# Kernel optimization log

Measured on AMD Instinct MI355X. Metric: run time of the kernel, lower is better.

## Reference

```python
import jax, jax.numpy as jnp
import numpy as np

A, B, M, H, NMOL = 100000, 200000, 50000, 128, 4000
DEPTH = 5
MAX_NB = 8


def setup_inputs() -> dict:
    key = jax.random.key(0)
    ks = jax.random.split(key, 10)
    fatoms = jax.random.normal(ks[0], (A, 35), dtype=jnp.float32)
    fbonds = jax.random.normal(ks[1], (B, 40), dtype=jnp.float32)
    # index 0 of the combined message table is the zero padding message
    tree_message = jax.random.normal(ks[2], (M, H), dtype=jnp.float32).at[0].set(0.0)
    agraph = jax.random.randint(ks[3], (A, MAX_NB), 0, M + B, dtype=jnp.int32)
    bgraph = jax.random.randint(ks[4], (B, MAX_NB), 0, M + B, dtype=jnp.int32)
    mol_id = jnp.sort(jax.random.randint(ks[5], (A,), 0, NMOL, dtype=jnp.int32))
    W_i = jax.random.normal(ks[6], (40, H), dtype=jnp.float32) * 0.05
    W_h = jax.random.normal(ks[7], (H, H), dtype=jnp.float32) * 0.05
    W_o = jax.random.normal(ks[8], (35 + H, H), dtype=jnp.float32) * 0.05
    b_o = jax.random.normal(ks[9], (H,), dtype=jnp.float32) * 0.05
    return {"fatoms": fatoms, "fbonds": fbonds, "tree_message": tree_message,
            "agraph": agraph, "bgraph": bgraph, "mol_id": mol_id,
            "W_i": W_i, "W_h": W_h, "W_o": W_o, "b_o": b_o, "n_mols": NMOL}


def reference(fatoms, fbonds, tree_message, agraph, bgraph, mol_id, W_i, W_h, W_o, b_o, n_mols):
    binput = fbonds @ W_i                      # [B, H]
    graph_message = jax.nn.relu(binput)        # [B, H]
    for _ in range(DEPTH - 1):
        message = jnp.concatenate([tree_message, graph_message], axis=0)  # [M+B, H]
        nei = jnp.take(message, bgraph, axis=0).sum(axis=1)               # [B, H]
        graph_message = jax.nn.relu(binput + nei @ W_h)
    message = jnp.concatenate([tree_message, graph_message], axis=0)
    nei_a = jnp.take(message, agraph, axis=0).sum(axis=1)                 # [A, H]
    ainput = jnp.concatenate([fatoms, nei_a], axis=1)                     # [A, 35+H]
    atom_hiddens = jax.nn.relu(ainput @ W_o + b_o)                        # [A, H]
    sums = jax.ops.segment_sum(atom_hiddens, mol_id, num_segments=n_mols)
    counts = jax.ops.segment_sum(jnp.ones((atom_hiddens.shape[0],), dtype=atom_hiddens.dtype),
                                 mol_id, num_segments=n_mols)
    mol_vecs = sums / jnp.maximum(counts, 1.0)[:, None]                   # [n_mols, H]
    return mol_vecs
```

## Files before the change

### kernel.cpp

```cpp
#include <hip/hip_runtime.h>
#include <hip/hip_bf16.h>

#define AN 100000
#define BN 200000
#define MN 50000
#define HD 128
#define NMOL 4000
#define MAXNB 8
#define BSZ 24576

typedef unsigned short u16;
typedef unsigned int   u32;
typedef unsigned char  u8;
typedef float f32x4 __attribute__((ext_vector_type(4)));
typedef float f32x2 __attribute__((ext_vector_type(2)));
typedef short s16x8 __attribute__((ext_vector_type(8)));

__device__ __forceinline__ u16 f2bf(float x) {
    u32 u = __float_as_uint(x);
    return (u16)((u + 0x7fffu + ((u >> 16) & 1u)) >> 16);
}
__device__ __forceinline__ float bf2f(u16 x) { return __uint_as_float((u32)x << 16); }

__device__ __forceinline__ s16x8 zero8() { return (s16x8){0, 0, 0, 0, 0, 0, 0, 0}; }

__device__ __forceinline__ s16x8 pack44(float4 a, float4 b) {
    union { uint4 u; s16x8 s; } r;
    r.u.x = (u32)f2bf(a.x) | ((u32)f2bf(a.y) << 16);
    r.u.y = (u32)f2bf(a.z) | ((u32)f2bf(a.w) << 16);
    r.u.z = (u32)f2bf(b.x) | ((u32)f2bf(b.y) << 16);
    r.u.w = (u32)f2bf(b.z) | ((u32)f2bf(b.w) << 16);
    return r.s;
}

#if defined(__has_builtin)
#if __has_builtin(__builtin_amdgcn_cvt_pk_f32_fp8) && __has_builtin(__builtin_amdgcn_cvt_pk_fp8_f32)
#define HW_FP8 1
#endif
#endif

__device__ __forceinline__ void fp8x4_to_f32(u32 w, float* o) {
#ifdef HW_FP8
    f32x2 a = __builtin_amdgcn_cvt_pk_f32_fp8((int)w, false);
    f32x2 b = __builtin_amdgcn_cvt_pk_f32_fp8((int)w, true);
    o[0] = a.x; o[1] = a.y; o[2] = b.x; o[3] = b.y;
#else
#pragma unroll
    for (int i = 0; i < 4; ++i) {
        u32 b8 = (w >> (i * 8)) & 0xffu;
        u32 s = (b8 >> 7) & 1u, em = b8 & 0x7fu;
        float v;
        if (em < 8u) v = (float)em * 0.001953125f;
        else v = __uint_as_float((((em >> 3) + 120u) << 23) | ((em & 7u) << 20));
        o[i] = s ? -v : v;
    }
#endif
}

__device__ __forceinline__ u32 f32_1_to_fp8_sw(float x) {
    u32 s = (__float_as_uint(x) >> 31) << 7;
    float ax = fabsf(x);
    if (ax >= 448.f) return s | 0x7e;
    u32 b = __float_as_uint(ax);
    int e = (int)(b >> 23) - 127;
    if (e < -6) {
        float t = ax * 512.0f;
        u32 m = (u32)(t + 0.5f);
        if (m > 8u) m = 8u;
        return s | m;
    }
    u32 mant = b & 0x7fffffu;
    u32 keep = mant >> 20;
    u32 rest = mant & 0xfffffu;
    u32 rnd = (rest > 0x80000u) || (rest == 0x80000u && (keep & 1u));
    keep += rnd;
    u32 ee = (u32)(e + 7);
    if (keep == 8u) { keep = 0u; ee++; }
    if (ee >= 16u || (ee == 15u && keep == 7u)) return s | 0x7e;
    return s | (ee << 3) | keep;
}

__device__ __forceinline__ u32 f32x4_to_fp8(float a, float b, float c, float d) {
#ifdef HW_FP8
    int r = __builtin_amdgcn_cvt_pk_fp8_f32(a, b, 0, false);
    r = __builtin_amdgcn_cvt_pk_fp8_f32(c, d, r, true);
    return (u32)r;
#else
    return f32_1_to_fp8_sw(a) | (f32_1_to_fp8_sw(b) << 8) |
           (f32_1_to_fp8_sw(c) << 16) | (f32_1_to_fp8_sw(d) << 24);
#endif
}

__global__ __launch_bounds__(256) void k_prep(const float* __restrict__ tree,
                                              u16* __restrict__ tree_bf,
                                              const float* __restrict__ W_h,
                                              const float* __restrict__ W_i,
                                              const float* __restrict__ W_o,
                                              const float* __restrict__ b_o,
                                              u16* __restrict__ Bit,
                                              u16* __restrict__ Bat,
                                              const int* __restrict__ mol_id,
                                              float* __restrict__ counts,
                                              const float* __restrict__ fbonds,
                                              u16* __restrict__ fbp,
                                              const int* __restrict__ bgraph,
                                              int* __restrict__ bgd,
                                              int bgd_end) {
    int blk = blockIdx.x, tid = threadIdx.x;
    if (blk < 6250) {
        int i = blk * 256 + tid;
        const float4 v = ((const float4*)tree)[i];
        uint2 r;
        r.x = (u32)f2bf(v.x) | ((u32)f2bf(v.y) << 16);
        r.y = (u32)f2bf(v.z) | ((u32)f2bf(v.w) << 16);
        ((uint2*)tree_bf)[i] = r;
    } else if (blk < 6442) {
        int i = (blk - 6250) * 256 + tid;
        int which = (i >= BSZ);
        int e = which ? i - BSZ : i;
        int j = e & 7, lane = (e >> 3) & 63, nt = (e >> 9) & 7, kt = e >> 12;
        int k = kt * 32 + (lane >> 4) * 8 + j;
        int n = nt * 16 + (lane & 15);
        if (!which) {
            float v = (k < 128) ? W_h[k * 128 + n] : ((k < 168) ? W_i[(k - 128) * 128 + n] : 0.f);
            Bit[e] = f2bf(v);
        } else {
            float v = (k < 128) ? W_o[(35 + k) * 128 + n]
                    : (k < 163) ? W_o[(k - 128) * 128 + n]
                    : (k == 163) ? b_o[n] : 0.f;
            Bat[e] = f2bf(v);
        }
    } else if (blk < 6458) {
        int m = (blk - 6442) * 256 + tid;
        if (m < NMOL) {
            int lo = 0, hi = AN;
            while (lo < hi) { int mid = (lo + hi) >> 1; if (mol_id[mid] < m) lo = mid + 1; else hi = mid; }
            int s = lo; lo = 0; hi = AN;
            while (lo < hi) { int mid = (lo + hi) >> 1; if (mol_id[mid] < m + 1) lo = mid + 1; else hi = mid; }
            counts[m] = (float)(lo - s);
        }
    } else if (blk < bgd_end) {
        int q = (blk - 6458) * 256 + tid;
        if (q < 400000) {
            int4 v = ((const int4*)bgraph)[q];
            v.x = (v.x >= MN) ? v.x : 0;
            v.y = (v.y >= MN) ? v.y : 0;
            v.z = (v.z >= MN) ? v.z : 0;
            v.w = (v.w >= MN) ? v.w : 0;
            ((int4*)bgd)[q] = v;
        }
    } else {
        int q = (blk - bgd_end) * 256 + tid;
        if (q < 2000000) {
            const float4 v = ((const float4*)fbonds)[q];
            uint2 r;
            r.x = (u32)f2bf(v.x) | ((u32)f2bf(v.y) << 16);
            r.y = (u32)f2bf(v.z) | ((u32)f2bf(v.w) << 16);
            ((uint2*)fbp)[q] = r;
        }
    }
}

#define LDA 136

__device__ __forceinline__ void fb_frags_pk(const u16* __restrict__ fbp, int b, int aq,
                                            s16x8& lo, s16x8& hi) {
    const uint4* f4 = (const uint4*)fbp;
    uint4 v = f4[(size_t)b * 5 + aq];
    lo = *(const s16x8*)&v;
    if (aq == 0) {
        uint4 w = f4[(size_t)b * 5 + 4];
        hi = *(const s16x8*)&w;
    } else hi = zero8();
}

__device__ __forceinline__ void fb_frags_f32(const float* __restrict__ fbonds, int b, int aq,
                                             s16x8& lo, s16x8& hi) {
    const float4* f4 = (const float4*)(fbonds + (size_t)b * 40);
    float4 x = f4[aq * 2], y = f4[aq * 2 + 1];
    lo = pack44(x, y);
    if (aq == 0) {
        float4 p = f4[8], q = f4[9];
        hi = pack44(p, q);
    } else hi = zero8();
}

__device__ __forceinline__ void acc_bf16(const uint4& v, float* a) {
    a[0] += __uint_as_float(v.x << 16);
    a[1] += __uint_as_float(v.x & 0xffff0000u);
    a[2] += __uint_as_float(v.y << 16);
    a[3] += __uint_as_float(v.y & 0xffff0000u);
    a[4] += __uint_as_float(v.z << 16);
    a[5] += __uint_as_float(v.z & 0xffff0000u);
    a[6] += __uint_as_float(v.w << 16);
    a[7] += __uint_as_float(v.w & 0xffff0000u);
}

__device__ __forceinline__ void pack_row(u16 (*sA)[LDA], int row, int l, const float* a) {
    uint4 r;
    r.x = (u32)f2bf(a[0]) | ((u32)f2bf(a[1]) << 16);
    r.y = (u32)f2bf(a[2]) | ((u32)f2bf(a[3]) << 16);
    r.z = (u32)f2bf(a[4]) | ((u32)f2bf(a[5]) << 16);
    r.w = (u32)f2bf(a[6]) | ((u32)f2bf(a[7]) << 16);
    *(uint4*)&sA[row][l * 8] = r;
}

__device__ __forceinline__ void gather16(u16 (*sA)[LDA], const int (*sidx)[MAXNB],
                                         const u16* __restrict__ tree_bf,
                                         const u16* __restrict__ tin, int tid) {
    int l = tid & 15, tb = tid >> 4;
#pragma unroll
    for (int pp = 0; pp < 2; ++pp) {
        int r0 = tb + (2 * pp) * 16;
        int r1 = tb + (2 * pp + 1) * 16;
        uint4 v[2][8];
#pragma unroll
        for (int j = 0; j < 8; ++j) {
            int idx = sidx[r0][j];
            const u16* base = (idx < MN) ? tree_bf + (size_t)idx * HD
                                         : tin + (size_t)(idx - MN) * HD;
            v[0][j] = ((const uint4*)base)[l];
        }
#pragma unroll
        for (int j = 0; j < 8; ++j) {
            int idx = sidx[r1][j];
            const u16* base = (idx < MN) ? tree_bf + (size_t)idx * HD
                                         : tin + (size_t)(idx - MN) * HD;
            v[1][j] = ((const uint4*)base)[l];
        }
#pragma unroll
        for (int h = 0; h < 2; ++h) {
            float a[8] = {0.f, 0.f, 0.f, 0.f, 0.f, 0.f, 0.f, 0.f};
#pragma unroll
            for (int j = 0; j < 8; ++j) acc_bf16(v[h][j], a);
            pack_row(sA, h == 0 ? r0 : r1, l, a);
        }
    }
}

__device__ __forceinline__ void gather_tree(u16 (*sA)[LDA], const int (*sidx)[MAXNB],
                                            const u16* __restrict__ tree_bf, int tid) {
    int l = tid & 15, tb = tid >> 4;
#pragma unroll
    for (int pp = 0; pp < 2; ++pp) {
        int r0 = tb + (2 * pp) * 16;
        int r1 = tb + (2 * pp + 1) * 16;
        uint4 v[2][8];
#pragma unroll
        for (int j = 0; j < 8; ++j) {
            int idx = sidx[r0][j];
            uint4 w = {0u, 0u, 0u, 0u};
            if (idx) w = ((const uint4*)(tree_bf + (size_t)idx * HD))[l];
            v[0][j] = w;
        }
#pragma unroll
        for (int j = 0; j < 8; ++j) {
            int idx = sidx[r1][j];
            uint4 w = {0u, 0u, 0u, 0u};
            if (idx) w = ((const uint4*)(tree_bf + (size_t)idx * HD))[l];
            v[1][j] = w;
        }
#pragma unroll
        for (int h = 0; h < 2; ++h) {
            float a[8] = {0.f, 0.f, 0.f, 0.f, 0.f, 0.f, 0.f, 0.f};
#pragma unroll
            for (int j = 0; j < 8; ++j) acc_bf16(v[h][j], a);
            pack_row(sA, h == 0 ? r0 : r1, l, a);
        }
    }
}

__device__ __forceinline__ void gather_fp8(u16 (*sA)[LDA], const int (*sidx)[MAXNB],
                                           const u8* __restrict__ tin, int tid) {
    int l = tid & 15, tb = tid >> 4;
#pragma unroll
    for (int pp = 0; pp < 2; ++pp) {
        int r0 = tb + (2 * pp) * 16;
        int r1 = tb + (2 * pp + 1) * 16;
        uint2 v[2][8];
#pragma unroll
        for (int j = 0; j < 8; ++j) {
            int idx = sidx[r0][j];
            uint2 w = {0u, 0u};
            if (idx) w = *((const uint2*)(tin + (size_t)(idx - MN) * HD) + l);
            v[0][j] = w;
        }
#pragma unroll
        for (int j = 0; j < 8; ++j) {
            int idx = sidx[r1][j];
            uint2 w = {0u, 0u};
            if (idx) w = *((const uint2*)(tin + (size_t)(idx - MN) * HD) + l);
            v[1][j] = w;
        }
#pragma unroll
        for (int h = 0; h < 2; ++h) {
            float a[8] = {0.f, 0.f, 0.f, 0.f, 0.f, 0.f, 0.f, 0.f};
#pragma unroll
            for (int j = 0; j < 8; ++j) {
                float t[4];
                fp8x4_to_f32(v[h][j].x, t);
                a[0] += t[0]; a[1] += t[1]; a[2] += t[2]; a[3] += t[3];
                fp8x4_to_f32(v[h][j].y, t);
                a[4] += t[0]; a[5] += t[1]; a[6] += t[2]; a[7] += t[3];
            }
            pack_row(sA, h == 0 ? r0 : r1, l, a);
        }
    }
}

__device__ __forceinline__ void gather_mixed(u16 (*sA)[LDA], const int (*sidx)[MAXNB],
                                             const u16* __restrict__ tree_bf,
                                             const u8* __restrict__ dyn, int tid) {
    int l = tid & 15, tb = tid >> 4;
#pragma unroll
    for (int pp = 0; pp < 4; ++pp) {
        int r = tb + pp * 16;
        uint4 v[8]; int id[8];
#pragma unroll
        for (int j = 0; j < 8; ++j) {
            int idx = sidx[r][j];
            id[j] = idx;
            uint4 w = {0u, 0u, 0u, 0u};
            if (idx >= MN) {
                uint2 t = *((const uint2*)(dyn + (size_t)(idx - MN) * HD) + l);
                w.x = t.x; w.y = t.y;
            } else if (idx) {
                w = ((const uint4*)(tree_bf + (size_t)idx * HD))[l];
            }
            v[j] = w;
        }
        float a[8] = {0.f, 0.f, 0.f, 0.f, 0.f, 0.f, 0.f, 0.f};
#pragma unroll
        for (int j = 0; j < 8; ++j) {
            if (id[j] >= MN) {
                float t[4];
                fp8x4_to_f32(v[j].x, t);
                a[0] += t[0]; a[1] += t[1]; a[2] += t[2]; a[3] += t[3];
                fp8x4_to_f32(v[j].y, t);
                a[4] += t[0]; a[5] += t[1]; a[6] += t[2]; a[7] += t[3];
            } else {
                acc_bf16(v[j], a);
            }
        }
        pack_row(sA, r, l, a);
    }
}

__device__ __forceinline__ void store_tile_fp8(const u16 (*sA)[LDA], u8* __restrict__ dst,
                                               int b0, int tid) {
#pragma unroll
    for (int s = 0; s < 4; ++s) {
        int e = tid + s * 256;
        int row = e >> 4, seg = e & 15;
        uint4 w = *(const uint4*)&sA[row][seg * 8];
        float f0 = fminf(__uint_as_float(w.x << 16), 448.f);
        float f1 = fminf(__uint_as_float(w.x & 0xffff0000u), 448.f);
        float f2 = fminf(__uint_as_float(w.y << 16), 448.f);
        float f3 = fminf(__uint_as_float(w.y & 0xffff0000u), 448.f);
        float f4 = fminf(__uint_as_float(w.z << 16), 448.f);
        float f5 = fminf(__uint_as_float(w.z & 0xffff0000u), 448.f);
        float f6 = fminf(__uint_as_float(w.w << 16), 448.f);
        float f7 = fminf(__uint_as_float(w.w & 0xffff0000u), 448.f);
        uint2 o;
        o.x = f32x4_to_fp8(f0, f1, f2, f3);
        o.y = f32x4_to_fp8(f4, f5, f6, f7);
        *((uint2*)(dst + (size_t)(b0 + row) * HD) + seg) = o;
    }
}

template <bool PK>
__global__ __launch_bounds__(256) void k_binput2(const float* __restrict__ fbonds,
                                                 const u16* __restrict__ fbp,
                                                 const u16* __restrict__ tree_bf,
                                                 const int* __restrict__ bgraph,
                                                 const u16* __restrict__ Bsw,
                                                 u8* __restrict__ g0,
                                                 u16* __restrict__ base2) {
    __shared__ __align__(16) u16 sA[64][LDA];
    __shared__ int sidx[64][MAXNB];
    int tid = threadIdx.x;
    int b0  = blockIdx.x * 64;

    for (int i = tid; i < 64 * MAXNB; i += 256) {
        int idx = bgraph[(size_t)(b0 + (i >> 3)) * MAXNB + (i & 7)];
        sidx[i >> 3][i & 7] = (idx < MN) ? idx : 0;
    }
    __syncthreads();
    gather_tree(sA, sidx, tree_bf, tid);
    __syncthreads();

    int lane = tid & 63, wv = tid >> 6;
    int am = lane & 15, aq = lane >> 4;
    s16x8 afr[6];
#pragma unroll
    for (int kt = 0; kt < 4; ++kt)
        afr[kt] = *(const s16x8*)&sA[wv * 16 + am][kt * 32 + aq * 8];
    int b = b0 + wv * 16 + am;
    if (PK) fb_frags_pk(fbp, b, aq, afr[4], afr[5]);
    else    fb_frags_f32(fbonds, b, aq, afr[4], afr[5]);

    const s16x8* B8 = (const s16x8*)Bsw;
    f32x4 acc[8];
#pragma unroll
    for (int nt = 0; nt < 8; ++nt) acc[nt] = (f32x4){0.f, 0.f, 0.f, 0.f};
#pragma unroll
    for (int kt = 4; kt < 6; ++kt)
#pragma unroll
        for (int nt = 0; nt < 8; ++nt) {
            s16x8 bfr = B8[(kt * 8 + nt) * 64 + lane];
            acc[nt] = __builtin_amdgcn_mfma_f32_16x16x32_bf16(afr[kt], bfr, acc[nt], 0, 0, 0);
        }
#pragma unroll
    for (int nt = 0; nt < 8; ++nt)
#pragma unroll
        for (int r = 0; r < 4; ++r)
            sA[wv * 16 + aq * 4 + r][nt * 16 + am] = f2bf(fmaxf(acc[nt][r], 0.f));
    __syncthreads();
    store_tile_fp8(sA, g0, b0, tid);
#pragma unroll
    for (int kt = 0; kt < 4; ++kt)
#pragma unroll
        for (int nt = 0; nt < 8; ++nt) {
            s16x8 bfr = B8[(kt * 8 + nt) * 64 + lane];
            acc[nt] = __builtin_amdgcn_mfma_f32_16x16x32_bf16(afr[kt], bfr, acc[nt], 0, 0, 0);
        }
    __syncthreads();
#pragma unroll
    for (int nt = 0; nt < 8; ++nt)
#pragma unroll
        for (int r = 0; r < 4; ++r)
            sA[wv * 16 + aq * 4 + r][nt * 16 + am] = f2bf(acc[nt][r]);
    __syncthreads();
#pragma unroll
    for (int s = 0; s < 4; ++s) {
        int e = tid + s * 256;
        int row = e >> 4, seg = e & 15;
        *(uint4*)&base2[((size_t)b0 + row) * HD + seg * 8] = *(const uint4*)&sA[row][seg * 8];
    }
}

__global__ __launch_bounds__(256) void k_iter_fold(const u8* __restrict__ tin,
                                                   const u16* __restrict__ base2,
                                                   const int* __restrict__ bgd,
                                                   const u16* __restrict__ Bsw,
                                                   u8* __restrict__ tout) {
    __shared__ __align__(16) u16 sA[64][LDA];
    __shared__ int sidx[64][MAXNB];
    int tid = threadIdx.x;
    int b0  = blockIdx.x * 64;

    for (int i = tid; i < 64 * MAXNB; i += 256)
        sidx[i >> 3][i & 7] = bgd[(size_t)(b0 + (i >> 3)) * MAXNB + (i & 7)];
    __syncthreads();

    gather_fp8(sA, sidx, tin, tid);

    int lane = tid & 63, wv = tid >> 6;
    int am = lane & 15, aq = lane >> 4;
    f32x4 acc[8];
    {
        const u16* b2 = base2 + (size_t)(b0 + wv * 16 + aq * 4) * HD + am;
#pragma unroll
        for (int r = 0; r < 4; ++r)
#pragma unroll
            for (int nt = 0; nt < 8; ++nt)
                acc[nt][r] = bf2f(b2[(size_t)r * HD + nt * 16]);
    }
    __syncthreads();

    s16x8 afr[4];
#pragma unroll
    for (int kt = 0; kt < 4; ++kt)
        afr[kt] = *(const s16x8*)&sA[wv * 16 + am][kt * 32 + aq * 8];
    const s16x8* B8 = (const s16x8*)Bsw;
#pragma unroll
    for (int kt = 0; kt < 4; ++kt)
#pragma unroll
        for (int nt = 0; nt < 8; ++nt) {
            s16x8 bfr = B8[(kt * 8 + nt) * 64 + lane];
            acc[nt] = __builtin_amdgcn_mfma_f32_16x16x32_bf16(afr[kt], bfr, acc[nt], 0, 0, 0);
        }
#pragma unroll
    for (int nt = 0; nt < 8; ++nt)
#pragma unroll
        for (int r = 0; r < 4; ++r)
            sA[wv * 16 + aq * 4 + r][nt * 16 + am] = f2bf(fmaxf(acc[nt][r], 0.f));
    __syncthreads();
    store_tile_fp8(sA, tout, b0, tid);
}

template <bool PK>
__global__ __launch_bounds__(256) void k_binput_mfma(const float* __restrict__ fbonds,
                                                     const u16* __restrict__ fbp,
                                                     const u16* __restrict__ Bsw,
                                                     u16* __restrict__ g0) {
    __shared__ __align__(16) u16 sA[64][LDA];
    int tid = threadIdx.x;
    int b0  = blockIdx.x * 64;
    int lane = tid & 63, wv = tid >> 6;
    int am = lane & 15, aq = lane >> 4;
    int b = b0 + wv * 16 + am;
    s16x8 afr[2];
    if (PK) fb_frags_pk(fbp, b, aq, afr[0], afr[1]);
    else    fb_frags_f32(fbonds, b, aq, afr[0], afr[1]);
    f32x4 acc[8];
#pragma unroll
    for (int nt = 0; nt < 8; ++nt) acc[nt] = (f32x4){0.f, 0.f, 0.f, 0.f};
    const s16x8* B8 = (const s16x8*)Bsw;
#pragma unroll
    for (int kt = 0; kt < 2; ++kt)
#pragma unroll
        for (int nt = 0; nt < 8; ++nt) {
            s16x8 bfr = B8[((4 + kt) * 8 + nt) * 64 + lane];
            acc[nt] = __builtin_amdgcn_mfma_f32_16x16x32_bf16(afr[kt], bfr, acc[nt], 0, 0, 0);
        }
#pragma unroll
    for (int nt = 0; nt < 8; ++nt)
#pragma unroll
        for (int r = 0; r < 4; ++r)
            sA[wv * 16 + aq * 4 + r][nt * 16 + am] = f2bf(fmaxf(acc[nt][r], 0.f));
    __syncthreads();
#pragma unroll
    for (int s = 0; s < 4; ++s) {
        int e = tid + s * 256;
        int row = e >> 4, seg = e & 15;
        *(uint4*)&g0[((size_t)b0 + row) * HD + seg * 8] = *(const uint4*)&sA[row][seg * 8];
    }
}

template <bool PK>
__global__ __launch_bounds__(256) void k_iter_mfma(const u16* __restrict__ tree_bf,
                                                   const u16* __restrict__ tin,
                                                   const float* __restrict__ fbonds,
                                                   const u16* __restrict__ fbp,
                                                   const int* __restrict__ bgraph,
                                                   const u16* __restrict__ Bsw,
                                                   u16* __restrict__ tout) {
    __shared__ __align__(16) u16 sA[64][LDA];
    __shared__ int sidx[64][MAXNB];
    int tid = threadIdx.x;
    int b0  = blockIdx.x * 64;

    for (int i = tid; i < 64 * MAXNB; i += 256)
        sidx[i >> 3][i & 7] = bgraph[(size_t)(b0 + (i >> 3)) * MAXNB + (i & 7)];
    __syncthreads();

    gather16(sA, sidx, tree_bf, tin, tid);
    __syncthreads();

    int lane = tid & 63, wv = tid >> 6;
    int am = lane & 15, aq = lane >> 4;
    s16x8 afr[6];
#pragma unroll
    for (int kt = 0; kt < 4; ++kt)
        afr[kt] = *(const s16x8*)&sA[wv * 16 + am][kt * 32 + aq * 8];
    int b = b0 + wv * 16 + am;
    if (PK) fb_frags_pk(fbp, b, aq, afr[4], afr[5]);
    else    fb_frags_f32(fbonds, b, aq, afr[4], afr[5]);
    f32x4 acc[8];
#pragma unroll
    for (int nt = 0; nt < 8; ++nt) acc[nt] = (f32x4){0.f, 0.f, 0.f, 0.f};
    const s16x8* B8 = (const s16x8*)Bsw;
#pragma unroll
    for (int kt = 0; kt < 6; ++kt)
#pragma unroll
        for (int nt = 0; nt < 8; ++nt) {
            s16x8 bfr = B8[(kt * 8 + nt) * 64 + lane];
            acc[nt] = __builtin_amdgcn_mfma_f32_16x16x32_bf16(afr[kt], bfr, acc[nt], 0, 0, 0);
        }
#pragma unroll
    for (int nt = 0; nt < 8; ++nt)
#pragma unroll
        for (int r = 0; r < 4; ++r)
            sA[wv * 16 + aq * 4 + r][nt * 16 + am] = f2bf(fmaxf(acc[nt][r], 0.f));
    __syncthreads();
#pragma unroll
    for (int s = 0; s < 4; ++s) {
        int e = tid + s * 256;
        int row = e >> 4, seg = e & 15;
        *(uint4*)&tout[((size_t)b0 + row) * HD + seg * 8] = *(const uint4*)&sA[row][seg * 8];
    }
}

template <bool F8>
__global__ __launch_bounds__(256) void k_atom_mfma(const u16* __restrict__ tree_bf,
                                                   const void* __restrict__ gfin,
                                                   const float* __restrict__ fatoms,
                                                   const int* __restrict__ agraph,
                                                   const int* __restrict__ mol_id,
                                                   const u16* __restrict__ Bsw,
                                                   float* __restrict__ sums) {
    __shared__ __align__(16) u16 sA[64][LDA];
    __shared__ int sidx[64][MAXNB];
    __shared__ int smol[64];
    int tid = threadIdx.x;
    int a0  = blockIdx.x * 64;

    for (int i = tid; i < 64 * MAXNB; i += 256) {
        int a = a0 + (i >> 3);
        sidx[i >> 3][i & 7] = (a < AN) ? agraph[(size_t)a * MAXNB + (i & 7)] : 0;
    }
    if (tid < 64) smol[tid] = (a0 + tid < AN) ? mol_id[a0 + tid] : -1;
    __syncthreads();
    if (F8) gather_mixed(sA, sidx, tree_bf, (const u8*)gfin, tid);
    else    gather16(sA, sidx, tree_bf, (const u16*)gfin, tid);
    __syncthreads();

    int lane = tid & 63, wv = tid >> 6;
    int am = lane & 15, aq = lane >> 4;
    s16x8 afr[6];
#pragma unroll
    for (int kt = 0; kt < 4; ++kt)
        afr[kt] = *(const s16x8*)&sA[wv * 16 + am][kt * 32 + aq * 8];
    {
        int a = a0 + wv * 16 + am;
        float f[8] = {0.f, 0.f, 0.f, 0.f, 0.f, 0.f, 0.f, 0.f};
        if (a < AN) {
            const float* fr = fatoms + (size_t)a * 35;
#pragma unroll
            for (int j = 0; j < 8; ++j) f[j] = fr[aq * 8 + j];
        }
        union { uint4 u; s16x8 s; } r4;
        r4.u.x = (u32)f2bf(f[0]) | ((u32)f2bf(f[1]) << 16);
        r4.u.y = (u32)f2bf(f[2]) | ((u32)f2bf(f[3]) << 16);
        r4.u.z = (u32)f2bf(f[4]) | ((u32)f2bf(f[5]) << 16);
        r4.u.w = (u32)f2bf(f[6]) | ((u32)f2bf(f[7]) << 16);
        afr[4] = r4.s;
        if (aq == 0) {
            float g0 = 0.f, g1 = 0.f, g2 = 0.f, g3 = 0.f;
            if (a < AN) {
                const float* fr = fatoms + (size_t)a * 35;
                g0 = fr[32]; g1 = fr[33]; g2 = fr[34]; g3 = 1.f;
            }
            union { uint4 u; s16x8 s; } r5;
            r5.u.x = (u32)f2bf(g0) | ((u32)f2bf(g1) << 16);
            r5.u.y = (u32)f2bf(g2) | ((u32)f2bf(g3) << 16);
            r5.u.z = 0u; r5.u.w = 0u;
            afr[5] = r5.s;
        } else afr[5] = zero8();
    }

    f32x4 acc[8];
#pragma unroll
    for (int nt = 0; nt < 8; ++nt) acc[nt] = (f32x4){0.f, 0.f, 0.f, 0.f};
    const s16x8* B8 = (const s16x8*)Bsw;
#pragma unroll
    for (int kt = 0; kt < 6; ++kt)
#pragma unroll
        for (int nt = 0; nt < 8; ++nt) {
            s16x8 bfr = B8[(kt * 8 + nt) * 64 + lane];
            acc[nt] = __builtin_amdgcn_mfma_f32_16x16x32_bf16(afr[kt], bfr, acc[nt], 0, 0, 0);
        }
#pragma unroll
    for (int nt = 0; nt < 8; ++nt)
#pragma unroll
        for (int r = 0; r < 4; ++r)
            sA[wv * 16 + aq * 4 + r][nt * 16 + am] = f2bf(fmaxf(acc[nt][r], 0.f));
    __syncthreads();

    {
        int c = tid & 127, half = tid >> 7;
        int base = half * 32;
        float run = 0.f;
        int cur = smol[base];
        for (int r = 0; r < 32; ++r) {
            int row = base + r;
            int mv = smol[row];
            if (mv != cur) {
                if (cur >= 0) atomicAdd(&sums[(size_t)cur * HD + c], run);
                run = 0.f; cur = mv;
            }
            run += __uint_as_float((u32)sA[row][c] << 16);
        }
        if (cur >= 0) atomicAdd(&sums[(size_t)cur * HD + c], run);
    }
}

__global__ __launch_bounds__(256) void k_div(const float* __restrict__ sums,
                                             const float* __restrict__ counts,
                                             float* __restrict__ out) {
    int i = blockIdx.x * 256 + threadIdx.x;
    if (i < NMOL * HD) out[i] = sums[i] / fmaxf(counts[i >> 7], 1.f);
}

extern "C" void kernel_launch(void* const* d_in, const int* in_sizes, int n_in,
                              void* d_out, int out_size, void* d_ws, size_t ws_size,
                              hipStream_t stream) {
    const float* fatoms = (const float*)d_in[0];
    const float* fbonds = (const float*)d_in[1];
    const float* tree   = (const float*)d_in[2];
    const int*   agraph = (const int*)d_in[3];
    const int*   bgraph = (const int*)d_in[4];
    const int*   mol_id = (const int*)d_in[5];
    const float* W_i    = (const float*)d_in[6];
    const float* W_h    = (const float*)d_in[7];
    const float* W_o    = (const float*)d_in[8];
    const float* b_o    = (const float*)d_in[9];
    float* out = (float*)d_out;

    size_t tbl   = (size_t)BN * HD;
    size_t treeN = (size_t)MN * HD;
    size_t fbN   = (size_t)BN * 40;
    size_t redN  = (size_t)(NMOL * HD + NMOL);
    size_t edgeN = (size_t)BN * MAXNB;

    size_t need_base = (2 * tbl + treeN + 2 * BSZ) * 2 + redN * 4;
    size_t need_pack = need_base + fbN * 2;
    size_t need_fold = need_pack + tbl * 2 + edgeN * 4;

    if (ws_size < need_base) {
        hipMemsetAsync(d_out, 0, (size_t)out_size * sizeof(float), stream);
        return;
    }
    bool pk   = (ws_size >= need_pack);
    bool fold = (ws_size >= need_fold);

    u16* t0      = (u16*)d_ws;
    u16* t1      = t0 + tbl;
    u16* tree_bf = t1 + tbl;
    u16* Bit     = tree_bf + treeN;
    u16* Bat     = Bit + BSZ;
    u16* fbp     = pk ? (Bat + BSZ) : nullptr;
    u16* base2   = fold ? (fbp + fbN) : nullptr;
    int* bgd     = fold ? (int*)(base2 + tbl) : nullptr;
    float* sums  = (float*)(fold ? (void*)(bgd + edgeN)
                          : pk   ? (void*)(fbp + fbN)
                                 : (void*)(Bat + BSZ));
    float* counts = sums + (size_t)NMOL * HD;

    hipMemsetAsync(sums, 0, (size_t)NMOL * HD * sizeof(float), stream);

    int bgd_end = fold ? 6458 + 1563 : 6458;
    int prep_grid = bgd_end + (pk ? 7813 : 0);
    k_prep<<<prep_grid, 256, 0, stream>>>(tree, tree_bf, W_h, W_i, W_o, b_o,
                                          Bit, Bat, mol_id, counts, fbonds, fbp,
                                          bgraph, bgd, bgd_end);

    if (fold) {
        u8* f0 = (u8*)t0;
        u8* f1 = (u8*)t1;
        k_binput2<true><<<BN / 64, 256, 0, stream>>>(fbonds, fbp, tree_bf, bgraph,
                                                     Bit, f0, base2);
        u8* cur = f0;
        u8* nxt = f1;
        for (int it = 0; it < 4; ++it) {
            k_iter_fold<<<BN / 64, 256, 0, stream>>>(cur, base2, bgd, Bit, nxt);
            u8* t = cur; cur = nxt; nxt = t;
        }
        k_atom_mfma<true><<<(AN + 63) / 64, 256, 0, stream>>>(tree_bf, cur, fatoms, agraph,
                                                              mol_id, Bat, sums);
    } else {
        u16* cur = t0;
        u16* nxt = t1;
        if (pk)
            k_binput_mfma<true><<<BN / 64, 256, 0, stream>>>(fbonds, fbp, Bit, t0);
        else
            k_binput_mfma<false><<<BN / 64, 256, 0, stream>>>(fbonds, fbp, Bit, t0);
        for (int it = 0; it < 4; ++it) {
            if (pk)
                k_iter_mfma<true><<<BN / 64, 256, 0, stream>>>(tree_bf, cur, fbonds, fbp,
                                                               bgraph, Bit, nxt);
            else
                k_iter_mfma<false><<<BN / 64, 256, 0, stream>>>(tree_bf, cur, fbonds, fbp,
                                                                bgraph, Bit, nxt);
            u16* t = cur; cur = nxt; nxt = t;
        }
        k_atom_mfma<false><<<(AN + 63) / 64, 256, 0, stream>>>(tree_bf, cur, fatoms, agraph,
                                                               mol_id, Bat, sums);
    }
    k_div<<<(NMOL * HD) / 256, 256, 0, stream>>>(sums, counts, out);
}
```

Before: 397.7 us.

## Store base2 in MFMA-fragment layout and widen fp8/bf16 gather loads

```diff
diff --git a/kernel.cpp b/kernel.cpp
--- a/kernel.cpp
+++ b/kernel.cpp
@@ -242,69 +242,63 @@
                                             const u16* __restrict__ tree_bf, int tid) {
     int l = tid & 15, tb = tid >> 4;
 #pragma unroll
-    for (int pp = 0; pp < 2; ++pp) {
-        int r0 = tb + (2 * pp) * 16;
-        int r1 = tb + (2 * pp + 1) * 16;
-        uint4 v[2][8];
+    for (int pp = 0; pp < 4; ++pp) {
+        int r = tb + pp * 16;
+        uint4 v[8];
 #pragma unroll
         for (int j = 0; j < 8; ++j) {
-            int idx = sidx[r0][j];
+            int idx = sidx[r][j];
             uint4 w = {0u, 0u, 0u, 0u};
             if (idx) w = ((const uint4*)(tree_bf + (size_t)idx * HD))[l];
-            v[0][j] = w;
-        }
-#pragma unroll
-        for (int j = 0; j < 8; ++j) {
-            int idx = sidx[r1][j];
-            uint4 w = {0u, 0u, 0u, 0u};
-            if (idx) w = ((const uint4*)(tree_bf + (size_t)idx * HD))[l];
-            v[1][j] = w;
-        }
-#pragma unroll
-        for (int h = 0; h < 2; ++h) {
-            float a[8] = {0.f, 0.f, 0.f, 0.f, 0.f, 0.f, 0.f, 0.f};
-#pragma unroll
-            for (int j = 0; j < 8; ++j) acc_bf16(v[h][j], a);
-            pack_row(sA, h == 0 ? r0 : r1, l, a);
-        }
+            v[j] = w;
+        }
+        float a[8] = {0.f, 0.f, 0.f, 0.f, 0.f, 0.f, 0.f, 0.f};
+#pragma unroll
+        for (int j = 0; j < 8; ++j) acc_bf16(v[j], a);
+        pack_row(sA, r, l, a);
     }
 }
 
 __device__ __forceinline__ void gather_fp8(u16 (*sA)[LDA], const int (*sidx)[MAXNB],
                                            const u8* __restrict__ tin, int tid) {
-    int l = tid & 15, tb = tid >> 4;
+    int l = tid & 7, tb = tid >> 3;
 #pragma unroll
     for (int pp = 0; pp < 2; ++pp) {
-        int r0 = tb + (2 * pp) * 16;
-        int r1 = tb + (2 * pp + 1) * 16;
-        uint2 v[2][8];
+        int r = tb + pp * 32;
+        uint4 v[8];
 #pragma unroll
         for (int j = 0; j < 8; ++j) {
-            int idx = sidx[r0][j];
-            uint2 w = {0u, 0u};
-            if (idx) w = *((const uint2*)(tin + (size_t)(idx - MN) * HD) + l);
-            v[0][j] = w;
-        }
+            int idx = sidx[r][j];
+            uint4 w = {0u, 0u, 0u, 0u};
+            if (idx) w = *((const uint4*)(tin + (size_t)(idx - MN) * HD) + l);
+            v[j] = w;
+        }
+        float a[16];
+#pragma unroll
+        for (int i = 0; i < 16; ++i) a[i] = 0.f;
 #pragma unroll
         for (int j = 0; j < 8; ++j) {
-            int idx = sidx[r1][j];
-            uint2 w = {0u, 0u};
-            if (idx) w = *((const uint2*)(tin + (size_t)(idx - MN) * HD) + l);
-            v[1][j] = w;
-        }
-#pragma unroll
-        for (int h = 0; h < 2; ++h) {
-            float a[8] = {0.f, 0.f, 0.f, 0.f, 0.f, 0.f, 0.f, 0.f};
-#pragma unroll
-            for (int j = 0; j < 8; ++j) {
-                float t[4];
-                fp8x4_to_f32(v[h][j].x, t);
-                a[0] += t[0]; a[1] += t[1]; a[2] += t[2]; a[3] += t[3];
-                fp8x4_to_f32(v[h][j].y, t);
-                a[4] += t[0]; a[5] += t[1]; a[6] += t[2]; a[7] += t[3];
-            }
-            pack_row(sA, h == 0 ? r0 : r1, l, a);
-        }
+            float t[4];
+            fp8x4_to_f32(v[j].x, t);
+            a[0] += t[0];  a[1] += t[1];  a[2] += t[2];  a[3] += t[3];
+            fp8x4_to_f32(v[j].y, t);
+            a[4] += t[0];  a[5] += t[1];  a[6] += t[2];  a[7] += t[3];
+            fp8x4_to_f32(v[j].z, t);
+            a[8] += t[0];  a[9] += t[1];  a[10] += t[2]; a[11] += t[3];
+            fp8x4_to_f32(v[j].w, t);
+            a[12] += t[0]; a[13] += t[1]; a[14] += t[2]; a[15] += t[3];
+        }
+        uint4 w0, w1;
+        w0.x = (u32)f2bf(a[0])  | ((u32)f2bf(a[1])  << 16);
+        w0.y = (u32)f2bf(a[2])  | ((u32)f2bf(a[3])  << 16);
+        w0.z = (u32)f2bf(a[4])  | ((u32)f2bf(a[5])  << 16);
+        w0.w = (u32)f2bf(a[6])  | ((u32)f2bf(a[7])  << 16);
+        w1.x = (u32)f2bf(a[8])  | ((u32)f2bf(a[9])  << 16);
+        w1.y = (u32)f2bf(a[10]) | ((u32)f2bf(a[11]) << 16);
+        w1.z = (u32)f2bf(a[12]) | ((u32)f2bf(a[13]) << 16);
+        w1.w = (u32)f2bf(a[14]) | ((u32)f2bf(a[15]) << 16);
+        *(uint4*)&sA[r][l * 16]     = w0;
+        *(uint4*)&sA[r][l * 16 + 8] = w1;
     }
 }
 
@@ -424,18 +418,17 @@
             s16x8 bfr = B8[(kt * 8 + nt) * 64 + lane];
             acc[nt] = __builtin_amdgcn_mfma_f32_16x16x32_bf16(afr[kt], bfr, acc[nt], 0, 0, 0);
         }
-    __syncthreads();
-#pragma unroll
-    for (int nt = 0; nt < 8; ++nt)
-#pragma unroll
-        for (int r = 0; r < 4; ++r)
-            sA[wv * 16 + aq * 4 + r][nt * 16 + am] = f2bf(acc[nt][r]);
-    __syncthreads();
-#pragma unroll
-    for (int s = 0; s < 4; ++s) {
-        int e = tid + s * 256;
-        int row = e >> 4, seg = e & 15;
-        *(uint4*)&base2[((size_t)b0 + row) * HD + seg * 8] = *(const uint4*)&sA[row][seg * 8];
+    {
+        uint4* dst = (uint4*)(base2 + ((size_t)(blockIdx.x * 256 + tid)) * 32);
+#pragma unroll
+        for (int q = 0; q < 4; ++q) {
+            uint4 w;
+            w.x = (u32)f2bf(acc[2 * q][0])     | ((u32)f2bf(acc[2 * q][1]) << 16);
+            w.y = (u32)f2bf(acc[2 * q][2])     | ((u32)f2bf(acc[2 * q][3]) << 16);
+            w.z = (u32)f2bf(acc[2 * q + 1][0]) | ((u32)f2bf(acc[2 * q + 1][1]) << 16);
+            w.w = (u32)f2bf(acc[2 * q + 1][2]) | ((u32)f2bf(acc[2 * q + 1][3]) << 16);
+            dst[q] = w;
+        }
     }
 }
 
@@ -455,19 +448,22 @@
 
     gather_fp8(sA, sidx, tin, tid);
 
+    f32x4 acc[8];
+    {
+        const uint4* b2 = (const uint4*)(base2 + ((size_t)(blockIdx.x * 256 + tid)) * 32);
+#pragma unroll
+        for (int q = 0; q < 4; ++q) {
+            uint4 w = b2[q];
+            acc[2 * q][0]     = bf2f((u16)w.x); acc[2 * q][1]     = bf2f((u16)(w.x >> 16));
+            acc[2 * q][2]     = bf2f((u16)w.y); acc[2 * q][3]     = bf2f((u16)(w.y >> 16));
+            acc[2 * q + 1][0] = bf2f((u16)w.z); acc[2 * q + 1][1] = bf2f((u16)(w.z >> 16));
+            acc[2 * q + 1][2] = bf2f((u16)w.w); acc[2 * q + 1][3] = bf2f((u16)(w.w >> 16));
+        }
+    }
+    __syncthreads();
+
     int lane = tid & 63, wv = tid >> 6;
     int am = lane & 15, aq = lane >> 4;
-    f32x4 acc[8];
-    {
-        const u16* b2 = base2 + (size_t)(b0 + wv * 16 + aq * 4) * HD + am;
-#pragma unroll
-        for (int r = 0; r < 4; ++r)
-#pragma unroll
-            for (int nt = 0; nt < 8; ++nt)
-                acc[nt][r] = bf2f(b2[(size_t)r * HD + nt * 16]);
-    }
-    __syncthreads();
-
     s16x8 afr[4];
 #pragma unroll
     for (int kt = 0; kt < 4; ++kt)
```

Measured after the change: 405.4 us. Within noise of the previous version (+1.9%).
